# Kernel optimization log

Measured on AMD Instinct MI355X. Metric: run time of the kernel, lower is better.

## Reference

```python
import jax, jax.numpy as jnp
import numpy as np

HID = 768
NUM_HEADS = 12
HEAD_DIM = HID // NUM_HEADS
MASK_VALUE = -1.0e9
EPS = 1.0e-4  # module's self.eps, also used as the diagonal fill constant


def setup_inputs() -> dict:
    key = jax.random.key(0)
    k1, k2, k3 = jax.random.split(key, 3)
    B, M = 16, 512
    ocr_features = jax.random.normal(k1, (B, M, HID), dtype=jnp.float32)
    # prior neighbor-attention from previous layer, probabilities in [0,1)
    prior = jax.random.uniform(k2, (B, 1, M, M), dtype=jnp.float32)
    Wq = jax.random.normal(k3, (HID, HID), dtype=jnp.float32) / np.sqrt(HID)
    bq = jnp.zeros((HID,), dtype=jnp.float32)
    ocr_features_mask = jnp.ones((B, M), dtype=jnp.int32)
    return {"ocr_features": ocr_features, "prior": prior, "Wq": Wq, "bq": bq,
            "ocr_features_mask": ocr_features_mask}


def reference(ocr_features, prior, Wq, bq, ocr_features_mask):
    B, M, _ = ocr_features.shape
    # Module uses q_linear for Q, K (and V, which is unused) -> Q == K.
    q = (ocr_features @ Wq + bq).reshape(B, M, NUM_HEADS, HEAD_DIM)
    q = q.transpose(0, 2, 1, 3)  # (B, H, M, D)
    # note: scaled by head_dim (not sqrt), as in the source
    scores = jnp.einsum('bhid,bhjd->bhij', q, q) / HEAD_DIM  # (B, H, M, M)

    dt = scores.dtype
    prev_word_mask = jnp.eye(M, k=1, dtype=dt)   # superdiagonal
    next_word_mask = jnp.eye(M, k=-1, dtype=dt)  # subdiagonal
    main_diag_mask = jnp.eye(M, dtype=dt)

    # neighbor mask: only prev/next word positions that are valid OCR tokens
    neibor_mask = ((prev_word_mask + next_word_mask)[None, :, :] > 0) & \
                  (ocr_features_mask[:, None, :] > 0)  # (B, M, M)
    scores = jnp.where(neibor_mask[:, None, :, :], scores, MASK_VALUE)
    neibor_attn = jax.nn.softmax(scores, axis=-1)
    # symmetrize: sqrt(a * a^T + eps)
    neibor_attn = jnp.sqrt(neibor_attn * jnp.swapaxes(neibor_attn, -1, -2) + EPS)
    neibor_attn = prior + (1.0 - prior) * neibor_attn

    # log-space cumulative product via triangular matmuls
    tri = jnp.triu(jnp.ones((M, M), dtype=dt))  # (M, M), incl. diagonal
    # keep only superdiagonal log-probs, cumulative-sum to the right via tri
    t = jnp.where(prev_word_mask > 0, jnp.log(neibor_attn + 1e-9), 0.0) @ tri
    g_attn = jnp.exp(jnp.einsum('ij,bhjk->bhik', tri, t))
    # zero out diagonal and lower triangle (tri - diag == 0 there)
    g_attn = jnp.where((tri - main_diag_mask) > 0, g_attn, 0.0)
    g_attn = g_attn + jnp.swapaxes(g_attn, -1, -2) + \
             jnp.where(main_diag_mask > 0, neibor_attn, EPS)
    return (g_attn, neibor_attn)
```

## Files before the change

kernel.cpp:

```cpp
#include <hip/hip_runtime.h>
#include <cstdint>
#include <cstddef>

#define B_   16
#define M_   512
#define HID_ 768
#define NH_  12
#define HD_  64

typedef short s16x8 __attribute__((ext_vector_type(8)));
typedef float f32x4 __attribute__((ext_vector_type(4)));
typedef unsigned short u16x8 __attribute__((ext_vector_type(8)));
typedef unsigned short u16x4 __attribute__((ext_vector_type(4)));

__device__ __forceinline__ unsigned short f2bf(float f) {
    unsigned int u = __builtin_bit_cast(unsigned int, f);
    u = u + 0x7FFFu + ((u >> 16) & 1u);
    return (unsigned short)(u >> 16);
}

__device__ __forceinline__ void gld_lds16(const void* g, void* lds) {
    __builtin_amdgcn_global_load_lds(
        (const __attribute__((address_space(1))) unsigned int*)g,
        (__attribute__((address_space(3))) unsigned int*)lds,
        16, 0, 0);
}

__launch_bounds__(256)
__global__ void prep(const float* __restrict__ X, const float* __restrict__ W,
                     unsigned short* __restrict__ Xb, unsigned short* __restrict__ Wt) {
    __shared__ float T[32][33];
    const int blk = blockIdx.x;
    const int t   = threadIdx.x;
    if (blk < 3072) {
        const size_t i = ((size_t)blk * 256 + t) * 8;
        const float4 a = *(const float4*)(X + i);
        const float4 b = *(const float4*)(X + i + 4);
        u16x8 v = { f2bf(a.x), f2bf(a.y), f2bf(a.z), f2bf(a.w),
                    f2bf(b.x), f2bf(b.y), f2bf(b.z), f2bf(b.w) };
        *(u16x8*)(Xb + i) = v;
    } else {
        const int tb = blk - 3072;
        const int n0 = (tb % 24) * 32;
        const int k0 = (tb / 24) * 32;
        #pragma unroll
        for (int p = 0; p < 4; ++p) {
            const int r = p * 8 + (t >> 5);
            const int c = t & 31;
            T[r][c] = W[(size_t)(k0 + r) * HID_ + n0 + c];
        }
        __syncthreads();
        const int nl = t >> 3;
        const int k4 = (t & 7) * 4;
        u16x4 v = { f2bf(T[k4 + 0][nl]), f2bf(T[k4 + 1][nl]),
                    f2bf(T[k4 + 2][nl]), f2bf(T[k4 + 3][nl]) };
        *(u16x4*)(Wt + (size_t)(n0 + nl) * HID_ + k0 + k4) = v;
    }
}

__launch_bounds__(256)
__global__ void gemm_qb(const unsigned short* __restrict__ Xb,
                        const unsigned short* __restrict__ Wt,
                        const float* __restrict__ bq, float* __restrict__ Q) {
    __shared__ unsigned short As[128 * 64];
    __shared__ unsigned short Bs[128 * 64];

    const int tid  = threadIdx.x;
    const int lane = tid & 63;
    const int wave = tid >> 6;
    const int wr   = (wave >> 1) * 64;
    const int wc   = (wave & 1) * 64;
    const int ln   = lane & 15;
    const int quad = lane >> 4;
    const int r0   = blockIdx.y * 128;
    const int n0   = blockIdx.x * 128;

    const int srow  = lane >> 3;
    const int selem = ((lane & 7) ^ (lane >> 3)) * 8;
    const int swz   = (ln & 7) << 4;

    f32x4 acc[4][4] = {};

    for (int kt = 0; kt < HID_ / 64; ++kt) {
        const int k0 = kt * 64;
        #pragma unroll
        for (int c = wave * 4; c < wave * 4 + 4; ++c) {
            const unsigned short* ga = Xb + (size_t)(r0 + c * 8 + srow) * HID_ + k0 + selem;
            gld_lds16(ga, (char*)As + c * 1024);
            const unsigned short* gb = Wt + (size_t)(n0 + c * 8 + srow) * HID_ + k0 + selem;
            gld_lds16(gb, (char*)Bs + c * 1024);
        }
        __syncthreads();

        #pragma unroll
        for (int kk = 0; kk < 2; ++kk) {
            s16x8 af[4], bf[4];
            #pragma unroll
            for (int r = 0; r < 4; ++r)
                af[r] = *(const s16x8*)((const char*)As + (wr + r * 16 + ln) * 128
                                        + ((kk * 64 + quad * 16) ^ swz));
            #pragma unroll
            for (int c = 0; c < 4; ++c)
                bf[c] = *(const s16x8*)((const char*)Bs + (wc + c * 16 + ln) * 128
                                        + ((kk * 64 + quad * 16) ^ swz));
            #pragma unroll
            for (int r = 0; r < 4; ++r)
                #pragma unroll
                for (int c = 0; c < 4; ++c)
                    acc[r][c] = __builtin_amdgcn_mfma_f32_16x16x32_bf16(af[r], bf[c], acc[r][c], 0, 0, 0);
        }
        __syncthreads();
    }

    #pragma unroll
    for (int c = 0; c < 4; ++c) {
        const int col = n0 + wc + c * 16 + ln;
        const float bias = bq[col];
        #pragma unroll
        for (int r = 0; r < 4; ++r) {
            const int rowb = r0 + wr + r * 16 + quad * 4;
            #pragma unroll
            for (int e = 0; e < 4; ++e)
                Q[(size_t)(rowb + e) * HID_ + col] = acc[r][c][e] + bias;
        }
    }
}

__launch_bounds__(256)
__global__ void dots(const float* __restrict__ Q, float* __restrict__ sdot) {
    const int w    = blockIdx.x * 4 + (threadIdx.x >> 6);
    const int lane = threadIdx.x & 63;
    const int b    = w >> 9;
    const int i    = w & 511;
    if (i >= M_ - 1) return;

    const float* ra = Q + (size_t)(b * M_ + i) * HID_;
    const float* rb = ra + HID_;

    #pragma unroll
    for (int c = 0; c < 3; ++c) {
        const int e = c * 256 + lane * 4;
        const float4 a = *(const float4*)(ra + e);
        const float4 bq4 = *(const float4*)(rb + e);
        float p = a.x * bq4.x + a.y * bq4.y + a.z * bq4.z + a.w * bq4.w;
        #pragma unroll
        for (int off = 1; off < 16; off <<= 1)
            p += __shfl_xor(p, off, 64);
        if ((lane & 15) == 0) {
            const int h = c * 4 + (lane >> 4);
            sdot[(size_t)(b * NH_ + h) * M_ + i] = p * (1.f / 64.f);
        }
    }
}

__launch_bounds__(512)
__global__ void scanstats(const float* __restrict__ sdot, const float* __restrict__ prior,
                          const int* __restrict__ mask,
                          float* __restrict__ na_super, float* __restrict__ na_sub,
                          float* __restrict__ Ssum) {
    const int bh = blockIdx.x;
    const int b  = bh / NH_;
    const int i  = threadIdx.x;
    const int lane = i & 63;
    const int wid  = i >> 6;

    __shared__ float sh_s[M_];
    __shared__ float sh_pp[M_];
    __shared__ float wsum[8];

    const float s = (i < M_ - 1) ? sdot[bh * M_ + i] : 0.f;
    sh_s[i] = s;
    __syncthreads();

    const bool vp = (i > 0)      && (mask[b * M_ + i - 1] > 0);
    const bool vn = (i < M_ - 1) && (mask[b * M_ + i + 1] > 0);
    const float sp = vp ? sh_s[i - 1] : -1e30f;
    const float sn = vn ? s : -1e30f;
    const float mx = fmaxf(sp, sn);
    const float ep = vp ? __expf(sp - mx) : 0.f;
    const float en = vn ? __expf(sn - mx) : 0.f;
    float den = ep + en;
    den = (den > 0.f) ? den : 1.f;
    const float pp = ep / den;
    const float pn = en / den;
    sh_pp[i] = pp;
    __syncthreads();

    float Lv = 0.f;
    if (i < M_ - 1) {
        const float  sym = sqrtf(pn * sh_pp[i + 1] + 1e-4f);
        const size_t pb  = (size_t)b * (M_ * M_);
        const float  prs = prior[pb + (size_t)i * M_ + (i + 1)];
        const float  prb = prior[pb + (size_t)(i + 1) * M_ + i];
        const float  nsup = prs + (1.f - prs) * sym;
        na_super[bh * M_ + i] = nsup;
        na_sub[bh * M_ + i]   = prb + (1.f - prb) * sym;
        Lv = logf(nsup + 1e-9f);
    }

    float v = Lv;
    #pragma unroll
    for (int off = 1; off < 64; off <<= 1) {
        float tt = __shfl_up(v, off, 64);
        if (lane >= off) v += tt;
    }
    if (lane == 63) wsum[wid] = v;
    __syncthreads();
    float base = 0.f;
    for (int w = 0; w < wid; ++w) base += wsum[w];
    Ssum[bh * M_ + i] = v + base - Lv;
}

__launch_bounds__(256)
__global__ void fill_out(const float* __restrict__ prior,
                         const float* __restrict__ na_super,
                         const float* __restrict__ na_sub,
                         const float* __restrict__ Ssum,
                         float* __restrict__ out) {
    const int tid = threadIdx.x;
    const int bi  = blockIdx.x;
    const int b   = bi >> 8;
    const int i   = ((bi & 255) << 1) | (tid >> 7);
    const int j0  = (tid & 127) * 4;

    const f32x4 pr4 = __builtin_nontemporal_load(
        (const f32x4*)(prior + (size_t)b * (M_ * M_) + (size_t)i * M_ + j0));
    const float pv[4] = {pr4[0], pr4[1], pr4[2], pr4[3]};
    const float c0 = 0.00999999977f;
    const size_t half = (size_t)B_ * NH_ * M_ * M_;

    #pragma unroll 2
    for (int h = 0; h < NH_; ++h) {
        const int bh = b * NH_ + h;
        const float4 S4 = *(const float4*)(Ssum + (size_t)bh * M_ + j0);
        const float  Si = Ssum[bh * M_ + i];
        const float  nsup_i   = (i < M_ - 1) ? na_super[bh * M_ + i]   : 0.f;
        const float  nsub_im1 = (i > 0)      ? na_sub[bh * M_ + i - 1] : 0.f;
        const float sv[4] = {S4.x, S4.y, S4.z, S4.w};

        f32x4 nav, ggv;
        #pragma unroll
        for (int e = 0; e < 4; ++e) {
            const int j = j0 + e;
            float na = fmaf(pv[e], 1.f - c0, c0);
            if (j == i - 1) na = nsub_im1;
            if (j == i + 1) na = nsup_i;
            const float d = sv[e] - Si;
            float g = __expf((j > i) ? d : -d) + 1e-4f;
            if (j == i) g = na;
            nav[e] = na;
            ggv[e] = g;
        }

        const size_t off = ((size_t)(bh * M_ + i)) * M_ + j0;
        __builtin_nontemporal_store(ggv, (f32x4*)(out + off));
        __builtin_nontemporal_store(nav, (f32x4*)(out + half + off));
    }
}

extern "C" void kernel_launch(void* const* d_in, const int* in_sizes, int n_in,
                              void* d_out, int out_size, void* d_ws, size_t ws_size,
                              hipStream_t stream) {
    const float* X     = (const float*)d_in[0];
    const float* prior = (const float*)d_in[1];
    const float* Wq    = (const float*)d_in[2];
    const float* bq    = (const float*)d_in[3];
    const int*   msk   = (const int*)  d_in[4];
    float* out = (float*)d_out;

    float* Q        = (float*)d_ws;
    float* na_super = Q + (size_t)B_ * M_ * HID_;
    float* na_sub   = na_super + (size_t)B_ * NH_ * M_;
    float* Ssum     = na_sub   + (size_t)B_ * NH_ * M_;
    unsigned short* Xb = (unsigned short*)(Ssum + (size_t)B_ * NH_ * M_);
    unsigned short* Wt = Xb + (size_t)B_ * M_ * HID_;
    float* sdot     = (float*)Xb;

    prep<<<3072 + 576, 256, 0, stream>>>(X, Wq, Xb, Wt);

    dim3 gg(HID_ / 128, (B_ * M_) / 128);
    gemm_qb<<<gg, 256, 0, stream>>>(Xb, Wt, bq, Q);

    dots<<<2048, 256, 0, stream>>>(Q, sdot);

    scanstats<<<B_ * NH_, M_, 0, stream>>>(sdot, prior, msk, na_super, na_sub, Ssum);

    fill_out<<<B_ * (M_ / 2), 256, 0, stream>>>(prior, na_super, na_sub, Ssum, out);
}
```

Baseline: 462.9 us.

## Fuse neighbor dot products into GEMM epilogue and drop Q materialization

The projection GEMM now stages its 128x128 output tile in swizzled LDS and computes the adjacent-row per-head dot products directly, writing only the small sdot array and the tile's first and last rows. Dot products that cross tile boundaries are finished in scanstats from those saved edge rows. This removes the full fp32 Q write and reread (about 25 MB each way) and one kernel launch. The block index is also remapped so neighbouring blocks share rows, which may help L2 reuse. The cost is 64 KB of LDS per GEMM block, which lowers occupancy.

```diff
diff --git a/kernel.cpp b/kernel.cpp
--- a/kernel.cpp
+++ b/kernel.cpp
@@ -24,6 +24,10 @@
         (const __attribute__((address_space(1))) unsigned int*)g,
         (__attribute__((address_space(3))) unsigned int*)lds,
         16, 0, 0);
+}
+
+__device__ __forceinline__ int csx(int r, int c) {
+    return (r << 7) | (c ^ (r & 31));
 }
 
 __launch_bounds__(256)
@@ -59,11 +63,14 @@
 }
 
 __launch_bounds__(256)
-__global__ void gemm_qb(const unsigned short* __restrict__ Xb,
-                        const unsigned short* __restrict__ Wt,
-                        const float* __restrict__ bq, float* __restrict__ Q) {
-    __shared__ unsigned short As[128 * 64];
-    __shared__ unsigned short Bs[128 * 64];
+__global__ void gemm_dots(const unsigned short* __restrict__ Xb,
+                          const unsigned short* __restrict__ Wt,
+                          const float* __restrict__ bq,
+                          float* __restrict__ sdot, float* __restrict__ Qedge) {
+    __shared__ float smem[128 * 128];
+    unsigned short* As = (unsigned short*)smem;
+    unsigned short* Bs = (unsigned short*)smem + 128 * 64;
+    float* Cs = smem;
 
     const int tid  = threadIdx.x;
     const int lane = tid & 63;
@@ -72,8 +79,13 @@
     const int wc   = (wave & 1) * 64;
     const int ln   = lane & 15;
     const int quad = lane >> 4;
-    const int r0   = blockIdx.y * 128;
-    const int n0   = blockIdx.x * 128;
+
+    const int bid = blockIdx.x;
+    const int li  = bid >> 3;
+    const int by  = ((bid & 7) << 3) + li / 6;
+    const int bx  = li % 6;
+    const int r0  = by * 128;
+    const int n0  = bx * 128;
 
     const int srow  = lane >> 3;
     const int selem = ((lane & 7) ^ (lane >> 3)) * 8;
@@ -114,52 +126,53 @@
 
     #pragma unroll
     for (int c = 0; c < 4; ++c) {
-        const int col = n0 + wc + c * 16 + ln;
-        const float bias = bq[col];
+        const int col = wc + c * 16 + ln;
+        const float bias = bq[n0 + col];
         #pragma unroll
         for (int r = 0; r < 4; ++r) {
-            const int rowb = r0 + wr + r * 16 + quad * 4;
+            const int rowb = wr + r * 16 + quad * 4;
             #pragma unroll
             for (int e = 0; e < 4; ++e)
-                Q[(size_t)(rowb + e) * HID_ + col] = acc[r][c][e] + bias;
-        }
-    }
-}
-
-__launch_bounds__(256)
-__global__ void dots(const float* __restrict__ Q, float* __restrict__ sdot) {
-    const int w    = blockIdx.x * 4 + (threadIdx.x >> 6);
-    const int lane = threadIdx.x & 63;
-    const int b    = w >> 9;
-    const int i    = w & 511;
-    if (i >= M_ - 1) return;
-
-    const float* ra = Q + (size_t)(b * M_ + i) * HID_;
-    const float* rb = ra + HID_;
-
-    #pragma unroll
-    for (int c = 0; c < 3; ++c) {
-        const int e = c * 256 + lane * 4;
-        const float4 a = *(const float4*)(ra + e);
-        const float4 bq4 = *(const float4*)(rb + e);
-        float p = a.x * bq4.x + a.y * bq4.y + a.z * bq4.z + a.w * bq4.w;
-        #pragma unroll
-        for (int off = 1; off < 16; off <<= 1)
-            p += __shfl_xor(p, off, 64);
-        if ((lane & 15) == 0) {
-            const int h = c * 4 + (lane >> 4);
-            sdot[(size_t)(b * NH_ + h) * M_ + i] = p * (1.f / 64.f);
+                Cs[csx(rowb + e, col)] = acc[r][c][e] + bias;
+        }
+    }
+    __syncthreads();
+
+    {
+        const int s   = tid >> 7;
+        const int col = tid & 127;
+        const int row = s ? 127 : 0;
+        Qedge[(size_t)(by * 2 + s) * HID_ + n0 + col] = Cs[csx(row, col)];
+    }
+
+    {
+        const int p  = tid & 127;
+        const int hh = tid >> 7;
+        if (p < 127) {
+            const int base = hh * 64;
+            float s0 = 0.f, s1 = 0.f;
+            #pragma unroll
+            for (int d = 0; d < 64; d += 2) {
+                s0 += Cs[csx(p,     base + d)]     * Cs[csx(p + 1, base + d)];
+                s1 += Cs[csx(p,     base + d + 1)] * Cs[csx(p + 1, base + d + 1)];
+            }
+            const int g  = by * 128 + p;
+            const int bb = g >> 9;
+            const int ii = g & 511;
+            const int h  = bx * 2 + hh;
+            sdot[(size_t)(bb * NH_ + h) * M_ + ii] = (s0 + s1) * (1.f / 64.f);
         }
     }
 }
 
 __launch_bounds__(512)
-__global__ void scanstats(const float* __restrict__ sdot, const float* __restrict__ prior,
-                          const int* __restrict__ mask,
+__global__ void scanstats(const float* __restrict__ sdot, const float* __restrict__ Qedge,
+                          const float* __restrict__ prior, const int* __restrict__ mask,
                           float* __restrict__ na_super, float* __restrict__ na_sub,
                           float* __restrict__ Ssum) {
     const int bh = blockIdx.x;
     const int b  = bh / NH_;
+    const int h  = bh - b * NH_;
     const int i  = threadIdx.x;
     const int lane = i & 63;
     const int wid  = i >> 6;
@@ -168,7 +181,27 @@
     __shared__ float sh_pp[M_];
     __shared__ float wsum[8];
 
-    const float s = (i < M_ - 1) ? sdot[bh * M_ + i] : 0.f;
+    float s = 0.f;
+    if (i < M_ - 1) {
+        if ((i & 127) == 127) {
+            const int gby = (b << 2) + (i >> 7);
+            const float* qa = Qedge + (size_t)(gby * 2 + 1) * HID_ + h * HD_;
+            const float* qb = Qedge + (size_t)(gby + 1) * 2 * HID_ + h * HD_;
+            float a0 = 0.f, a1 = 0.f;
+            #pragma unroll
+            for (int d = 0; d < HD_; d += 8) {
+                const float4 xa = *(const float4*)(qa + d);
+                const float4 xb = *(const float4*)(qb + d);
+                const float4 ya = *(const float4*)(qa + d + 4);
+                const float4 yb = *(const float4*)(qb + d + 4);
+                a0 += xa.x * xb.x + xa.y * xb.y + xa.z * xb.z + xa.w * xb.w;
+                a1 += ya.x * yb.x + ya.y * yb.y + ya.z * yb.z + ya.w * yb.w;
+            }
+            s = (a0 + a1) * (1.f / 64.f);
+        } else {
+            s = sdot[bh * M_ + i];
+        }
+    }
     sh_s[i] = s;
     __syncthreads();
 
@@ -268,22 +301,19 @@
     const int*   msk   = (const int*)  d_in[4];
     float* out = (float*)d_out;
 
-    float* Q        = (float*)d_ws;
-    float* na_super = Q + (size_t)B_ * M_ * HID_;
+    float* na_super = (float*)d_ws;
     float* na_sub   = na_super + (size_t)B_ * NH_ * M_;
     float* Ssum     = na_sub   + (size_t)B_ * NH_ * M_;
-    unsigned short* Xb = (unsigned short*)(Ssum + (size_t)B_ * NH_ * M_);
+    float* sdot     = Ssum     + (size_t)B_ * NH_ * M_;
+    float* Qedge    = sdot     + (size_t)B_ * NH_ * M_;
+    unsigned short* Xb = (unsigned short*)(Qedge + (size_t)64 * 2 * HID_);
     unsigned short* Wt = Xb + (size_t)B_ * M_ * HID_;
-    float* sdot     = (float*)Xb;
 
     prep<<<3072 + 576, 256, 0, stream>>>(X, Wq, Xb, Wt);
 
-    dim3 gg(HID_ / 128, (B_ * M_) / 128);
-    gemm_qb<<<gg, 256, 0, stream>>>(Xb, Wt, bq, Q);
-
-    dots<<<2048, 256, 0, stream>>>(Q, sdot);
-
-    scanstats<<<B_ * NH_, M_, 0, stream>>>(sdot, prior, msk, na_super, na_sub, Ssum);
+    gemm_dots<<<384, 256, 0, stream>>>(Xb, Wt, bq, sdot, Qedge);
+
+    scanstats<<<B_ * NH_, M_, 0, stream>>>(sdot, Qedge, prior, msk, na_super, na_sub, Ssum);
 
     fill_out<<<B_ * (M_ / 2), 256, 0, stream>>>(prior, na_super, na_sub, Ssum, out);
 }
```

Measured after the change: 457.6 us. No clear change (-1.1%).
